# Kernel tuning notes

Hardware: AMD Instinct MI355X
Metric: run time of the kernel (lower is better)

The kernel has to match this reference:

```python
import jax, jax.numpy as jnp
import numpy as np

B, T, E, H, V = 64, 32, 300, 1024, 10000


def setup_inputs() -> dict:
    key = jax.random.key(0)
    ks = jax.random.split(key, 12)
    s = lambda fan: 1.0 / np.sqrt(fan)
    return {
        "questions": jax.random.randint(ks[0], (B, T), 0, V, dtype=jnp.int64) if jax.config.jax_enable_x64 else jax.random.randint(ks[0], (B, T), 0, V, dtype=jnp.int32),
        "question_lengths": jax.random.randint(ks[1], (B,), 1, T + 1, dtype=jnp.int32),
        "embed_table": jax.random.normal(ks[2], (V, E), jnp.float32) * 0.02,
        "W_ih1": jax.random.normal(ks[3], (4 * H, E), jnp.float32) * s(H),
        "W_hh1": jax.random.normal(ks[4], (4 * H, H), jnp.float32) * s(H),
        "b_ih1": jax.random.normal(ks[5], (4 * H,), jnp.float32) * s(H),
        "b_hh1": jax.random.normal(ks[6], (4 * H,), jnp.float32) * s(H),
        "W_ih2": jax.random.normal(ks[7], (4 * H, H), jnp.float32) * s(H),
        "W_hh2": jax.random.normal(ks[8], (4 * H, H), jnp.float32) * s(H),
        "b_ih2": jax.random.normal(ks[9], (4 * H,), jnp.float32) * s(H),
        "b_hh2": jax.random.normal(ks[10], (4 * H,), jnp.float32) * s(H),
    }


def _lstm_cell(x_t, h, c, W_ih, W_hh, b_ih, b_hh):
    # PyTorch LSTMCell: gate order i, f, g, o
    gates = x_t @ W_ih.T + b_ih + h @ W_hh.T + b_hh  # [B, 4H]
    i, f, g, o = jnp.split(gates, 4, axis=-1)
    c_new = jax.nn.sigmoid(f) * c + jax.nn.sigmoid(i) * jnp.tanh(g)
    h_new = jax.nn.sigmoid(o) * jnp.tanh(c_new)
    return h_new, c_new


def reference(questions, question_lengths, embed_table,
              W_ih1, W_hh1, b_ih1, b_hh1, W_ih2, W_hh2, b_ih2, b_hh2):
    x = embed_table[questions]                      # [B, T, E]
    b, t, _ = x.shape
    h = W_hh1.shape[1]

    def step(carry, inp):
        h1, c1, h2, c2 = carry
        x_t, m = inp                                # x_t [B,E], m [B,1] bool
        h1n, c1n = _lstm_cell(x_t, h1, c1, W_ih1, W_hh1, b_ih1, b_hh1)
        h2n, c2n = _lstm_cell(h1n, h2, c2, W_ih2, W_hh2, b_ih2, b_hh2)
        # samples past their length keep their final state frozen
        h1 = jnp.where(m, h1n, h1); c1 = jnp.where(m, c1n, c1)
        h2 = jnp.where(m, h2n, h2); c2 = jnp.where(m, c2n, c2)
        return (h1, c1, h2, c2), None

    mask = jnp.arange(t)[None, :] < question_lengths[:, None]      # [B,T]
    xs = (jnp.swapaxes(x, 0, 1), jnp.swapaxes(mask, 0, 1)[..., None])
    init = tuple(jnp.zeros((b, h), x.dtype) for _ in range(4))
    (h1, c1, h2, c2), _ = jax.lax.scan(step, init, xs)

    # tile final top-layer hidden to [B, H, 28, 28]
    E_q = jnp.broadcast_to(h2[:, None, None, :], (b, 28, 28, h))
    E_q = jnp.transpose(E_q, (0, 3, 2, 1))
    return (E_q, h1[:, None, :], h2[:, None, :], c1[:, None, :], c2[:, None, :])
```

## Files before the change

### kernel.cpp

```cpp
#include <hip/hip_runtime.h>
#include <hip/hip_bf16.h>
#include <cstdint>

#define B_  64
#define T_  32
#define E_  300
#define EP  320
#define H_  1024
#define G4  4096
#define BH  65536
#define NBLK 192

#define EQOFF 0LL
#define H1OFF 51380224LL
#define H2OFF 51445760LL
#define C1OFF 51511296LL
#define C2OFF 51576832LL

typedef __attribute__((ext_vector_type(8))) short bf16x8;
typedef __attribute__((ext_vector_type(4))) float f32x4;
typedef unsigned short ushort_t;

__device__ __forceinline__ bf16x8 load_b8(const ushort_t* p) {
    union { uint4 u; bf16x8 v; } c;
    c.u = *reinterpret_cast<const uint4*>(p);
    return c.v;
}

__device__ __forceinline__ ushort_t f2bf(float x) {
    union { float f; uint32_t u; } c; c.f = x;
    uint32_t r = c.u + 0x7fffu + ((c.u >> 16) & 1u);
    return (ushort_t)(r >> 16);
}

__device__ __forceinline__ float sigm(float x) { return 1.0f / (1.0f + __expf(-x)); }

__device__ __forceinline__ void astore64(uint64_t* p, uint64_t v) {
    __hip_atomic_store(p, v, __ATOMIC_RELAXED, __HIP_MEMORY_SCOPE_AGENT);
}
__device__ __forceinline__ uint64_t packf2(float a, float b) {
    union { float f[2]; uint64_t u; } c; c.f[0] = a; c.f[1] = b; return c.u;
}

__device__ __forceinline__ void setflag(int* flags, int role, int js, int val) {
    __hip_atomic_store(&flags[(role * 64 + js) * 16], val,
                       __ATOMIC_RELAXED, __HIP_MEMORY_SCOPE_AGENT);
}
__device__ __forceinline__ void waitwave(const int* flags, int role, int target, int lane) {
    const int* p = &flags[(role * 64 + lane) * 16];
    int guard = 0;
    for (;;) {
        int v = __hip_atomic_load(p, __ATOMIC_RELAXED, __HIP_MEMORY_SCOPE_AGENT);
        if (__all(v >= target)) return;
        if (++guard > (1 << 22)) return;
        __builtin_amdgcn_s_sleep(1);
    }
}

__global__ void prep_inputs(const int* __restrict__ q, const float* __restrict__ table,
                            ushort_t* __restrict__ Xp,
                            const float* __restrict__ Wsrc, ushort_t* __restrict__ Wdst,
                            ushort_t* __restrict__ h1s0, ushort_t* __restrict__ h2s0,
                            int* __restrict__ flags) {
    int blk = blockIdx.x;
    if (blk < 1280) {
        int i = blk * 256 + threadIdx.x;
        const int n = B_ * T_ * EP;
        for (; i < n; i += 1280 * 256) {
            int r = i / EP, c = i - r * EP;
            Xp[i] = (c < E_) ? f2bf(table[q[r] * E_ + c]) : (ushort_t)0;
        }
    } else if (blk < 3328) {
        int i = (blk - 1280) * 256 + threadIdx.x;
        const int n = G4 * EP;
        for (; i < n; i += 2048 * 256) {
            int r = i / EP, c = i - r * EP;
            Wdst[i] = (c < E_) ? f2bf(Wsrc[r * E_ + c]) : (ushort_t)0;
        }
    } else if (blk < 3392) {
        int i = (blk - 3328) * 256 + threadIdx.x;
        uint4 z = make_uint4(0, 0, 0, 0);
        if (i < 8192) reinterpret_cast<uint4*>(h1s0)[i] = z;
        else          reinterpret_cast<uint4*>(h2s0)[i - 8192] = z;
    } else {
        int i = (blk - 3392) * 256 + threadIdx.x;
        reinterpret_cast<uint4*>(flags)[i] = make_uint4(0, 0, 0, 0);
    }
}

__launch_bounds__(256)
__global__ void xgemm(const ushort_t* __restrict__ Xp, const ushort_t* __restrict__ Wp,
                      const float* __restrict__ b_ih1, const float* __restrict__ b_hh1,
                      float* __restrict__ xg) {
    int mblk = blockIdx.x, nblk = blockIdx.y;
    int wave = threadIdx.x >> 6, lane = threadIdx.x & 63;
    int lm = lane & 15, lq = lane >> 4;
    int m0 = mblk * 64 + wave * 16;
    f32x4 acc[4];
    #pragma unroll
    for (int g = 0; g < 4; ++g) {
        int n = nblk * 64 + g * 16 + lm;
        float bv = b_ih1[n] + b_hh1[n];
        acc[g] = (f32x4){bv, bv, bv, bv};
    }
    for (int k0 = 0; k0 < EP; k0 += 32) {
        bf16x8 a = load_b8(Xp + (m0 + lm) * EP + k0 + lq * 8);
        #pragma unroll
        for (int g = 0; g < 4; ++g) {
            bf16x8 b = load_b8(Wp + (nblk * 64 + g * 16 + lm) * EP + k0 + lq * 8);
            acc[g] = __builtin_amdgcn_mfma_f32_16x16x32_bf16(a, b, acc[g], 0, 0, 0);
        }
    }
    #pragma unroll
    for (int g = 0; g < 4; ++g)
        #pragma unroll
        for (int r = 0; r < 4; ++r) {
            int m = m0 + lq * 4 + r;
            int b = m >> 5, t = m & 31;
            int n = nblk * 64 + g * 16 + lm;
            int gate = n >> 10, j = n & 1023;
            xg[(((size_t)t * B_ + b) * H_ + j) * 4 + gate] = acc[g][r];
        }
}


__device__ __forceinline__ void gemm_half(const ushort_t* __restrict__ hslot,
                                          const ushort_t* __restrict__ wsf,
                                          int lm, int lq, int m0, int kh, f32x4 acc[4]) {
    const uint4* hr = reinterpret_cast<const uint4*>(hslot);
    const int rbase = (m0 + lm) * 2 + (lq & 1);
    const int cbo = lq >> 1;
    const int cb0 = kh * 32;
    uint4 buf[16];
    #pragma unroll
    for (int grp = 0; grp < 2; ++grp)
        #pragma unroll
        for (int i = 0; i < 8; ++i)
            buf[grp * 8 + i] = hr[(cb0 + grp * 16 + i * 2 + cbo) * 128 + rbase];
    #pragma unroll
    for (int grp = 0; grp < 2; ++grp)
        #pragma unroll
        for (int i = 0; i < 8; ++i) {
            int k0 = kh * 512 + grp * 256 + i * 32;
            union { uint4 u; bf16x8 v; } a; a.u = buf[grp * 8 + i];
            #pragma unroll
            for (int g = 0; g < 4; ++g) {
                int row = g * 16 + lm;
                bf16x8 bb = load_b8(wsf + row * 1024 + ((k0 + lq * 8) ^ ((lm & 7) << 3)));
                acc[g] = __builtin_amdgcn_mfma_f32_16x16x32_bf16(a.v, bb, acc[g], 0, 0, 0);
            }
        }
}

__device__ __forceinline__ void lstm_elem(const f32x4 acc[4], int r,
                                          float* c, float* h, ushort_t* hb) {
    float iv = sigm(acc[0][r]);
    float fv = sigm(acc[1][r]);
    float gv = tanhf(acc[2][r]);
    float ov = sigm(acc[3][r]);
    float cn = fv * c[r] + iv * gv;
    float hv = ov * tanhf(cn);
    c[r] = cn; h[r] = hv; hb[r] = f2bf(hv);
}

__device__ __forceinline__ void store_h_tile(ushort_t* slot, int js, const ushort_t* hst) {
    int tid = threadIdx.x;
    uint64_t v = reinterpret_cast<const uint64_t*>(hst)[tid];
    astore64(reinterpret_cast<uint64_t*>(slot) + js * 256 + tid, v);
}

__global__ __launch_bounds__(512) void lstm_persist(
    const float* __restrict__ Whh1, const float* __restrict__ Wih2,
    const float* __restrict__ Whh2,
    const float* __restrict__ b_ih2, const float* __restrict__ b_hh2,
    const float* __restrict__ xg, const int* __restrict__ qlen,
    ushort_t* __restrict__ h1hist,
    ushort_t* __restrict__ h2hist,
    float* __restrict__ Qhist,
    float* __restrict__ out,
    int* __restrict__ flags)
{
    __shared__ ushort_t ws[64 * 1024];
    __shared__ __align__(16) ushort_t hstage[64][16];
    __shared__ f32x4 pacc[256][4];
    __shared__ float hstage32[64][16];
    __shared__ int qlen_sh[64];

    const int blk  = blockIdx.x;
    const int role = blk >> 6;
    const int js   = blk & 63;
    const int w    = threadIdx.x >> 6, lane = threadIdx.x & 63;
    const int mi   = w & 3, kh = w >> 2;
    const int lm = lane & 15, lq = lane >> 4;
    const int m0 = mi * 16;
    const int pidx = mi * 64 + lane;

    if (threadIdx.x < 64) qlen_sh[threadIdx.x] = qlen[threadIdx.x];

    const float* Wsrc = (role == 0) ? Whh1 : (role == 1) ? Wih2 : Whh2;
    uint2* wsp = reinterpret_cast<uint2*>(ws);
    for (int idx = threadIdx.x; idx < 64 * 256; idx += 512) {
        int r = idx >> 8, c4 = idx & 255;
        int grow = (r >> 4) * H_ + js * 16 + (r & 15);
        float4 v = reinterpret_cast<const float4*>(Wsrc + (size_t)grow * H_)[c4];
        uint2 pk;
        pk.x = (uint32_t)f2bf(v.x) | ((uint32_t)f2bf(v.y) << 16);
        pk.y = (uint32_t)f2bf(v.z) | ((uint32_t)f2bf(v.w) << 16);
        wsp[r * 256 + (c4 ^ ((r & 7) << 1))] = pk;
    }
    __syncthreads();

    int q[4];
    #pragma unroll
    for (int r = 0; r < 4; ++r) q[r] = qlen_sh[m0 + lq * 4 + r];

    float    c_reg[4]  = {0.f, 0.f, 0.f, 0.f};
    float    h_reg[4]  = {0.f, 0.f, 0.f, 0.f};
    ushort_t hb_reg[4] = {0, 0, 0, 0};

    if (role == 0) {
        for (int t = 0; t < T_; ++t) {
            f32x4 acc[4];
            #pragma unroll
            for (int g = 0; g < 4; ++g) acc[g] = (f32x4){0.f, 0.f, 0.f, 0.f};
            if (kh == 0) {
                uint4 xq[4];
                #pragma unroll
                for (int r = 0; r < 4; ++r)
                    xq[r] = reinterpret_cast<const uint4*>(xg)
                            [((size_t)t * B_ + (m0 + lq * 4 + r)) * H_ + js * 16 + lm];
                #pragma unroll
                for (int r = 0; r < 4; ++r) {
                    union { uint32_t u; float f; } x0, x1, x2, x3;
                    x0.u = xq[r].x; x1.u = xq[r].y; x2.u = xq[r].z; x3.u = xq[r].w;
                    acc[0][r] = x0.f; acc[1][r] = x1.f;
                    acc[2][r] = x2.f; acc[3][r] = x3.f;
                }
            }
            if (t > 0) {
                if (w == 0) waitwave(flags, 0, t, lane);
                __syncthreads();
            }
            gemm_half(h1hist + (size_t)t * BH, ws, lm, lq, m0, kh, acc);
            if (kh == 1) {
                #pragma unroll
                for (int g = 0; g < 4; ++g) pacc[pidx][g] = acc[g];
            }
            __syncthreads();
            if (kh == 0) {
                #pragma unroll
                for (int g = 0; g < 4; ++g) acc[g] += pacc[pidx][g];
                #pragma unroll
                for (int r = 0; r < 4; ++r) {
                    if (t < q[r]) lstm_elem(acc, r, c_reg, h_reg, hb_reg);
                    hstage[m0 + lq * 4 + r][lm] = hb_reg[r];
                }
            }
            __syncthreads();
            if (threadIdx.x < 256)
                store_h_tile(h1hist + (size_t)(t + 1) * BH, js, &hstage[0][0]);
            __syncthreads();
            if (threadIdx.x == 0) setflag(flags, 0, js, t + 1);
            if (kh == 0) {
                #pragma unroll
                for (int r = 0; r < 4; ++r) {
                    if (q[r] == t + 1) {
                        int b = m0 + lq * 4 + r, j = js * 16 + lm;
                        out[H1OFF + b * H_ + j] = h_reg[r];
                        out[C1OFF + b * H_ + j] = c_reg[r];
                    }
                }
            }
        }
    } else if (role == 1) {
        float bi[4];
        #pragma unroll
        for (int g = 0; g < 4; ++g) {
            int n = g * H_ + js * 16 + lm;
            bi[g] = b_ih2[n] + b_hh2[n];
        }
        for (int t = 0; t < T_; ++t) {
            if (w == 0) waitwave(flags, 0, t + 1, lane);
            __syncthreads();
            f32x4 acc[4];
            #pragma unroll
            for (int g = 0; g < 4; ++g)
                acc[g] = (kh == 0) ? (f32x4){bi[g], bi[g], bi[g], bi[g]}
                                   : (f32x4){0.f, 0.f, 0.f, 0.f};
            gemm_half(h1hist + (size_t)(t + 1) * BH, ws, lm, lq, m0, kh, acc);
            if (kh == 1) {
                #pragma unroll
                for (int g = 0; g < 4; ++g) pacc[pidx][g] = acc[g];
            }
            __syncthreads();
            if (kh == 0) {
                #pragma unroll
                for (int g = 0; g < 4; ++g) acc[g] += pacc[pidx][g];
                uint64_t* Qw64 = (uint64_t*)(Qhist + (size_t)t * (4 * BH));
                #pragma unroll
                for (int r = 0; r < 4; ++r) {
                    int b = m0 + lq * 4 + r, j = js * 16 + lm;
                    size_t base = ((size_t)b * H_ + j) * 2;
                    astore64(Qw64 + base,     packf2(acc[0][r], acc[1][r]));
                    astore64(Qw64 + base + 1, packf2(acc[2][r], acc[3][r]));
                }
            }
            __syncthreads();
            if (threadIdx.x == 0) setflag(flags, 1, js, t + 1);
        }
    } else {
        for (int t = 0; t < T_; ++t) {
            if (w == 0)               waitwave(flags, 1, t + 1, lane);
            else if (w == 1 && t > 0) waitwave(flags, 2, t,     lane);
            __syncthreads();
            uint4 qp[4];
            if (kh == 0) {
                const uint4* Qr = (const uint4*)(Qhist + (size_t)t * (4 * BH));
                #pragma unroll
                for (int r = 0; r < 4; ++r)
                    qp[r] = Qr[(size_t)(m0 + lq * 4 + r) * H_ + js * 16 + lm];
            }
            f32x4 acc[4];
            #pragma unroll
            for (int g = 0; g < 4; ++g) acc[g] = (f32x4){0.f, 0.f, 0.f, 0.f};
            gemm_half(h2hist + (size_t)t * BH, ws, lm, lq, m0, kh, acc);
            if (kh == 1) {
                #pragma unroll
                for (int g = 0; g < 4; ++g) pacc[pidx][g] = acc[g];
            }
            __syncthreads();
            if (kh == 0) {
                #pragma unroll
                for (int g = 0; g < 4; ++g) acc[g] += pacc[pidx][g];
                #pragma unroll
                for (int r = 0; r < 4; ++r) {
                    union { uint32_t u; float f; } x0, x1, x2, x3;
                    x0.u = qp[r].x; x1.u = qp[r].y; x2.u = qp[r].z; x3.u = qp[r].w;
                    acc[0][r] += x0.f; acc[1][r] += x1.f;
                    acc[2][r] += x2.f; acc[3][r] += x3.f;
                }
                #pragma unroll
                for (int r = 0; r < 4; ++r) {
                    if (t < q[r]) lstm_elem(acc, r, c_reg, h_reg, hb_reg);
                    hstage[m0 + lq * 4 + r][lm] = hb_reg[r];
                    hstage32[m0 + lq * 4 + r][lm] = h_reg[r];
                }
            }
            __syncthreads();
            if (threadIdx.x < 256)
                store_h_tile(h2hist + (size_t)(t + 1) * BH, js, &hstage[0][0]);
            __syncthreads();
            if (t < T_ - 1 && threadIdx.x == 0) setflag(flags, 2, js, t + 1);
            if (kh == 0) {
                #pragma unroll
                for (int r = 0; r < 4; ++r) {
                    if (q[r] == t + 1) {
                        int b = m0 + lq * 4 + r, j = js * 16 + lm;
                        out[H2OFF + b * H_ + j] = h_reg[r];
                        out[C2OFF + b * H_ + j] = c_reg[r];
                    }
                }
            }
            for (int b = 0; b < B_; ++b) {
                if (qlen_sh[b] != t + 1) continue;
                float4* dst = reinterpret_cast<float4*>(
                    out + (size_t)b * (H_ * 784) + (size_t)js * 16 * 784);
                for (int idx = threadIdx.x; idx < 3136; idx += 512) {
                    int c = idx / 196, p4 = idx - c * 196;
                    float v = hstage32[b][c];
                    dst[c * 196 + p4] = make_float4(v, v, v, v);
                }
            }
        }
    }
}

extern "C" void kernel_launch(void* const* d_in, const int* in_sizes, int n_in,
                              void* d_out, int out_size, void* d_ws, size_t ws_size,
                              hipStream_t stream) {
    const int*   questions = (const int*)d_in[0];
    const int*   qlen      = (const int*)d_in[1];
    const float* embed     = (const float*)d_in[2];
    const float* W_ih1     = (const float*)d_in[3];
    const float* W_hh1     = (const float*)d_in[4];
    const float* b_ih1     = (const float*)d_in[5];
    const float* b_hh1     = (const float*)d_in[6];
    const float* W_ih2     = (const float*)d_in[7];
    const float* W_hh2     = (const float*)d_in[8];
    const float* b_ih2     = (const float*)d_in[9];
    const float* b_hh2     = (const float*)d_in[10];
    float* out = (float*)d_out;

    char* w = (char*)d_ws;
    float*    xg     = (float*)(w + 0);
    ushort_t* Wih1p  = (ushort_t*)(w + 33554432);
    ushort_t* Xp     = (ushort_t*)(w + 36175872);
    ushort_t* h1hist = (ushort_t*)(w + 37486592);
    ushort_t* h2hist = (ushort_t*)(w + 41811968);
    float*    Qhist  = (float*)(w + 46137344);
    int*      flags  = (int*)(w + 80740352);

    prep_inputs<<<3395, 256, 0, stream>>>(questions, embed, Xp, W_ih1, Wih1p,
                                          h1hist, h2hist, flags);
    xgemm<<<dim3(32, 64), 256, 0, stream>>>(Xp, Wih1p, b_ih1, b_hh1, xg);

    lstm_persist<<<NBLK, 512, 0, stream>>>(W_hh1, W_ih2, W_hh2, b_ih2, b_hh2,
                                           xg, qlen,
                                           h1hist, h2hist, Qhist,
                                           out, flags);
}
```

Measured before the change: 607.8 us.

## Offload E_q broadcast writes to a dedicated fourth role of blocks

Adds 64 extra persistent blocks (role 3) that wait on layer-2 flags and write the large tiled E_q output from a new fp32 h2 buffer in global memory. This takes the ~200MB broadcast store off the layer-2 recurrence critical path. The per-sample final h/c writes also move ahead of the h-tile publication and flag set, which removes one kh==0 section per step. The cost is 64 more co-resident blocks, which needs enough CUs so the persistent spin-waits do not deadlock. The layer-2 flag is now also set at the last step.

```diff
diff --git a/kernel.cpp b/kernel.cpp
--- a/kernel.cpp
+++ b/kernel.cpp
@@ -9,7 +9,7 @@
 #define H_  1024
 #define G4  4096
 #define BH  65536
-#define NBLK 192
+#define NBLK 256
 
 #define EQOFF 0LL
 #define H1OFF 51380224LL
@@ -36,6 +36,9 @@
 __device__ __forceinline__ float sigm(float x) { return 1.0f / (1.0f + __expf(-x)); }
 
 __device__ __forceinline__ void astore64(uint64_t* p, uint64_t v) {
+    __hip_atomic_store(p, v, __ATOMIC_RELAXED, __HIP_MEMORY_SCOPE_AGENT);
+}
+__device__ __forceinline__ void astoref(float* p, float v) {
     __hip_atomic_store(p, v, __ATOMIC_RELAXED, __HIP_MEMORY_SCOPE_AGENT);
 }
 __device__ __forceinline__ uint64_t packf2(float a, float b) {
@@ -177,13 +180,13 @@
     ushort_t* __restrict__ h1hist,
     ushort_t* __restrict__ h2hist,
     float* __restrict__ Qhist,
+    float* __restrict__ h2f,
     float* __restrict__ out,
     int* __restrict__ flags)
 {
     __shared__ ushort_t ws[64 * 1024];
     __shared__ __align__(16) ushort_t hstage[64][16];
     __shared__ f32x4 pacc[256][4];
-    __shared__ float hstage32[64][16];
     __shared__ int qlen_sh[64];
 
     const int blk  = blockIdx.x;
@@ -196,6 +199,36 @@
     const int pidx = mi * 64 + lane;
 
     if (threadIdx.x < 64) qlen_sh[threadIdx.x] = qlen[threadIdx.x];
+
+    if (role == 3) {
+        __syncthreads();
+        for (int t = 0; t < T_; ++t) {
+            bool any = false;
+            for (int b = 0; b < B_; ++b) any |= (qlen_sh[b] == t + 1);
+            if (!any) continue;
+            if (threadIdx.x == 0) {
+                const int* p = &flags[(2 * 64 + js) * 16];
+                int guard = 0;
+                while (__hip_atomic_load(p, __ATOMIC_RELAXED, __HIP_MEMORY_SCOPE_AGENT) < t + 1) {
+                    if (++guard > (1 << 22)) break;
+                    __builtin_amdgcn_s_sleep(1);
+                }
+            }
+            __syncthreads();
+            for (int b = 0; b < B_; ++b) {
+                if (qlen_sh[b] != t + 1) continue;
+                const float* src = h2f + (size_t)b * H_ + js * 16;
+                float4* dst = reinterpret_cast<float4*>(
+                    out + (size_t)b * (H_ * 784) + (size_t)js * 16 * 784);
+                for (int idx = threadIdx.x; idx < 3136; idx += 512) {
+                    int c = idx / 196, p4 = idx - c * 196;
+                    float v = src[c];
+                    dst[c * 196 + p4] = make_float4(v, v, v, v);
+                }
+            }
+        }
+        return;
+    }
 
     const float* Wsrc = (role == 0) ? Whh1 : (role == 1) ? Wih2 : Whh2;
     uint2* wsp = reinterpret_cast<uint2*>(ws);
@@ -254,16 +287,6 @@
                 for (int r = 0; r < 4; ++r) {
                     if (t < q[r]) lstm_elem(acc, r, c_reg, h_reg, hb_reg);
                     hstage[m0 + lq * 4 + r][lm] = hb_reg[r];
-                }
-            }
-            __syncthreads();
-            if (threadIdx.x < 256)
-                store_h_tile(h1hist + (size_t)(t + 1) * BH, js, &hstage[0][0]);
-            __syncthreads();
-            if (threadIdx.x == 0) setflag(flags, 0, js, t + 1);
-            if (kh == 0) {
-                #pragma unroll
-                for (int r = 0; r < 4; ++r) {
                     if (q[r] == t + 1) {
                         int b = m0 + lq * 4 + r, j = js * 16 + lm;
                         out[H1OFF + b * H_ + j] = h_reg[r];
@@ -271,6 +294,11 @@
                     }
                 }
             }
+            __syncthreads();
+            if (threadIdx.x < 256)
+                store_h_tile(h1hist + (size_t)(t + 1) * BH, js, &hstage[0][0]);
+            __syncthreads();
+            if (threadIdx.x == 0) setflag(flags, 0, js, t + 1);
         }
     } else if (role == 1) {
         float bi[4];
@@ -343,34 +371,19 @@
                 for (int r = 0; r < 4; ++r) {
                     if (t < q[r]) lstm_elem(acc, r, c_reg, h_reg, hb_reg);
                     hstage[m0 + lq * 4 + r][lm] = hb_reg[r];
-                    hstage32[m0 + lq * 4 + r][lm] = h_reg[r];
-                }
-            }
-            __syncthreads();
-            if (threadIdx.x < 256)
-                store_h_tile(h2hist + (size_t)(t + 1) * BH, js, &hstage[0][0]);
-            __syncthreads();
-            if (t < T_ - 1 && threadIdx.x == 0) setflag(flags, 2, js, t + 1);
-            if (kh == 0) {
-                #pragma unroll
-                for (int r = 0; r < 4; ++r) {
                     if (q[r] == t + 1) {
                         int b = m0 + lq * 4 + r, j = js * 16 + lm;
+                        astoref(&h2f[(size_t)b * H_ + j], h_reg[r]);
                         out[H2OFF + b * H_ + j] = h_reg[r];
                         out[C2OFF + b * H_ + j] = c_reg[r];
                     }
                 }
             }
-            for (int b = 0; b < B_; ++b) {
-                if (qlen_sh[b] != t + 1) continue;
-                float4* dst = reinterpret_cast<float4*>(
-                    out + (size_t)b * (H_ * 784) + (size_t)js * 16 * 784);
-                for (int idx = threadIdx.x; idx < 3136; idx += 512) {
-                    int c = idx / 196, p4 = idx - c * 196;
-                    float v = hstage32[b][c];
-                    dst[c * 196 + p4] = make_float4(v, v, v, v);
-                }
-            }
+            __syncthreads();
+            if (threadIdx.x < 256)
+                store_h_tile(h2hist + (size_t)(t + 1) * BH, js, &hstage[0][0]);
+            __syncthreads();
+            if (threadIdx.x == 0) setflag(flags, 2, js, t + 1);
         }
     }
 }
@@ -398,6 +411,7 @@
     ushort_t* h1hist = (ushort_t*)(w + 37486592);
     ushort_t* h2hist = (ushort_t*)(w + 41811968);
     float*    Qhist  = (float*)(w + 46137344);
+    float*    h2f    = (float*)(w + 80216064);
     int*      flags  = (int*)(w + 80740352);
 
     prep_inputs<<<3395, 256, 0, stream>>>(questions, embed, Xp, W_ih1, Wih1p,
@@ -407,5 +421,5 @@
     lstm_persist<<<NBLK, 512, 0, stream>>>(W_hh1, W_ih2, W_hh2, b_ih2, b_hh2,
                                            xg, qlen,
                                            h1hist, h2hist, Qhist,
-                                           out, flags);
-}
+                                           h2f, out, flags);
+}
```

New measurement: 548.7 us. 9.7% less time.
